# Kernel optimization log

Hardware: AMD Instinct MI355X
Metric: run time of the kernel (lower is better)

## Reference

```python
import jax, jax.numpy as jnp
import numpy as np

B, S, C = 16, 1024, 8
V, D, E, H, R = 50257, 512, 8, 512, 32
F, RT, CD, Q = 1024, 512, 64, 128
EPS = 1e-6


def _normalize(x):
    n = jnp.maximum(jnp.linalg.norm(x, axis=-1, keepdims=True), EPS)
    return x / n


def _fake_quantize(x):
    # F.normalize then straight-through int8 quant on the unit vector
    xn = _normalize(x)
    q = jnp.clip(jnp.round(xn * 127.0), -127.0, 127.0)
    return xn + jax.lax.stop_gradient(q / 127.0 - xn)


def setup_inputs() -> dict:
    key = jax.random.key(0)
    ks = iter(jax.random.split(key, 64))

    def w(shape, s=0.02):
        return (jax.random.normal(next(ks), shape, dtype=jnp.float32) * s)

    inp = {}
    inp['prefix_tokens'] = jax.random.randint(next(ks), (B, S), 0, V, dtype=jnp.int32)
    inp['chunk_inputs'] = jax.random.randint(next(ks), (B, C), 0, V, dtype=jnp.int32)
    inp['chunk_targets'] = jax.random.randint(next(ks), (B, C), 0, V, dtype=jnp.int32)
    inp['next_chunk_tokens'] = jax.random.randint(next(ks), (B, C), 0, V, dtype=jnp.int32)

    inp['emb'] = w((V, D))
    # stacked per-expert AffineExpert params
    inp['Wa'] = w((E, D, H)); inp['ba'] = jnp.zeros((E, H), jnp.float32)
    inp['Wg'] = w((E, D, R)); inp['bg'] = jnp.zeros((E, R), jnp.float32)
    inp['Wu'] = w((E, D, H)); inp['bu'] = jnp.zeros((E, H), jnp.float32)
    inp['u_mat'] = w((E, H, R)); inp['v_mat'] = w((E, H, R))
    inp['Wp'] = w((E, H, F)); inp['bp'] = jnp.zeros((E, F), jnp.float32)
    # gate MLP
    inp['Wg1'] = w((D, D)); inp['bg1'] = jnp.zeros((D,), jnp.float32)
    inp['Wg2'] = w((D, E)); inp['bg2'] = jnp.zeros((E,), jnp.float32)
    # query / target / key / code-expansion / write-code
    inp['Wq'] = w((F, Q)); inp['bq'] = jnp.zeros((Q,), jnp.float32)
    inp['Wt1'] = w((2 * D, RT)); inp['bt1'] = jnp.zeros((RT,), jnp.float32)
    inp['Wt2'] = w((RT, RT)); inp['bt2'] = jnp.zeros((RT,), jnp.float32)
    inp['Wk'] = w((RT, Q)); inp['bk'] = jnp.zeros((Q,), jnp.float32)
    inp['Web'] = w((CD, RT))  # expansion_basis (no bias)
    inp['Wwc'] = w((F, CD)); inp['bwc'] = jnp.zeros((CD,), jnp.float32)
    # ctx MLP
    inp['Wc1'] = w((2 * F, F)); inp['bc1'] = jnp.zeros((F,), jnp.float32)
    inp['Wc2'] = w((F, F)); inp['bc2'] = jnp.zeros((F,), jnp.float32)
    # chunk decoder
    inp['chunk_pos'] = w((C, F))
    inp['Wci'] = w((D + F, F)); inp['bci'] = jnp.zeros((F,), jnp.float32)
    inp['Wm1'] = w((F, F)); inp['bm1'] = jnp.zeros((F,), jnp.float32)
    inp['Wm2'] = w((F, F)); inp['bm2'] = jnp.zeros((F,), jnp.float32)
    inp['Wlm'] = w((F, V)); inp['blm'] = jnp.zeros((V,), jnp.float32)
    return inp


def _expert_scan(x, Wa, ba, Wg, bg, Wu, bu, u_mat, v_mat):
    # x: [B,S,D]; precompute all per-step projections as one big GEMM each,
    # leading axis = time for lax.scan. A,U: [S,E,B,H], G: [S,E,B,R]
    A = jax.nn.sigmoid(jnp.einsum('bsd,edh->sebh', x, Wa) + ba[None, :, None, :])
    G = jnp.einsum('bsd,edr->sebr', x, Wg) + bg[None, :, None, :]
    U = jnp.einsum('bsd,edh->sebh', x, Wu) + bu[None, :, None, :]

    def step(state, inp):  # state: [E,B,H]
        a, g, u = inp
        low = jnp.einsum('ebh,ehr->ebr', state, v_mat) * g
        state = a * state + u + jnp.einsum('ebr,ehr->ebh', low, u_mat)
        return state, None

    state0 = jnp.zeros((E, B, H), x.dtype)
    state, _ = jax.lax.scan(step, state0, (A, G, U))
    return state  # [E,B,H]


def reference(prefix_tokens, chunk_inputs, chunk_targets, next_chunk_tokens,
              emb, Wa, ba, Wg, bg, Wu, bu, u_mat, v_mat, Wp, bp,
              Wg1, bg1, Wg2, bg2, Wq, bq, Wt1, bt1, Wt2, bt2, Wk, bk,
              Web, Wwc, bwc, Wc1, bc1, Wc2, bc2,
              chunk_pos, Wci, bci, Wm1, bm1, Wm2, bm2, Wlm, blm):
    # ---- encode_prefix ----
    prefix_emb = emb[prefix_tokens]                       # [B,S,D]
    summary = prefix_emb.mean(axis=1)                     # [B,D]
    gate_probs = jax.nn.softmax(jax.nn.silu(summary @ Wg1 + bg1) @ Wg2 + bg2, axis=-1)  # [B,E]
    states = _expert_scan(prefix_emb, Wa, ba, Wg, bg, Wu, bu, u_mat, v_mat)             # [E,B,H]
    proj = jnp.einsum('ebh,ehf->ebf', states, Wp) + bp[:, None, :]                       # [E,B,F]
    fused = jnp.einsum('ebf,be->bf', proj, gate_probs)    # [B,F]

    # ---- query / target / key ----
    q_st = _fake_quantize(fused @ Wq + bq)                # [B,Q]
    chunk_emb = emb[chunk_targets].mean(axis=1)           # [B,D]
    next_emb = emb[next_chunk_tokens].mean(axis=1)        # [B,D]
    t_in = jnp.concatenate([chunk_emb, next_emb], axis=-1)
    target_state = _normalize(jax.nn.silu(t_in @ Wt1 + bt1) @ Wt2 + bt2)  # [B,RT]
    target_k_st = _fake_quantize(target_state @ Wk + bk)  # [B,Q]

    # ---- read_context (bank=None path -> zero read) ----
    zero_read = jnp.zeros_like(fused)
    c_in = jnp.concatenate([fused, zero_read], axis=-1)
    ctx = jax.nn.silu(c_in @ Wc1 + bc1) @ Wc2 + bc2       # [B,F]

    # ---- write_from_ctx ----
    write_codes = ctx @ Wwc + bwc                         # [B,CD]
    write_state = _normalize(write_codes @ Web)           # [B,RT]
    write_k_st = _fake_quantize(write_state @ Wk + bk)    # [B,Q]

    # ---- decode_chunk ----
    tok = emb[chunk_inputs]                               # [B,C,D]
    ctx_rep = jnp.broadcast_to(ctx[:, None, :], (B, C, F))
    hidden = jnp.concatenate([tok, ctx_rep], axis=-1) @ Wci + bci + chunk_pos[None]  # [B,C,F]
    hidden = jax.nn.silu(hidden @ Wm1 + bm1) @ Wm2 + bm2
    logits = hidden @ Wlm + blm                           # [B,C,V]

    # ---- losses ----
    logp = jax.nn.log_softmax(logits, axis=-1)
    token_loss = -jnp.take_along_axis(logp, chunk_targets[..., None], axis=-1)[..., 0]
    loss_nll = token_loss.mean()
    sim = (q_st @ target_k_st.T) / jnp.sqrt(jnp.float32(Q))  # [B,B]
    return logits, loss_nll, sim, write_k_st
```

## Files before the change

kernel.cpp:

```cpp
#include <hip/hip_runtime.h>
#include <math.h>

constexpr int BB = 16;
constexpr int SS = 1024;
constexpr int CC = 8;
constexpr int VV = 50257;
constexpr int DD = 512;
constexpr int EE = 8;
constexpr int HH = 512;
constexpr int RR = 32;
constexpr int FF = 1024;
constexpr int RTd = 512;
constexpr int CDd = 64;
constexpr int QQ = 128;
constexpr int SCH = 128;

typedef short bf16x8 __attribute__((ext_vector_type(8)));
typedef float f32x4 __attribute__((ext_vector_type(4)));

__device__ __forceinline__ float sigm(float x){ return 1.0f/(1.0f+expf(-x)); }

__device__ __forceinline__ unsigned short f2bf(float f){
  unsigned int u = __float_as_uint(f);
  u += 0x7fff + ((u>>16)&1);
  return (unsigned short)(u>>16);
}
__device__ __forceinline__ float bf2f(unsigned short h){
  return __uint_as_float(((unsigned int)h)<<16);
}

__device__ __forceinline__ void gload16(unsigned short* l, const unsigned short* g){
  __builtin_amdgcn_global_load_lds(
      (const __attribute__((address_space(1))) unsigned int*)(g),
      (__attribute__((address_space(3))) unsigned int*)(l), 16, 0, 0);
}

__global__ __launch_bounds__(256) void gather_pack(const int* __restrict__ toks,
    const float* __restrict__ emb, unsigned short* __restrict__ xp){
  int id = blockIdx.x*256 + threadIdx.x;
  int b = id >> 17;
  int rem = id & 131071;
  int c = rem >> 14;
  int rem2 = rem & 16383;
  int kc = rem2 >> 10;
  int pb = rem2 & 1023;
  int row = pb >> 3, q = pb & 7;
  int v = q ^ (row & 7);
  int kq = v >> 1, h = v & 1;
  int tok = toks[b*SS + c*128 + row];
  const float* src = emb + (size_t)tok*DD + kc*32 + kq*8;
  unsigned short o[8];
  #pragma unroll
  for (int j=0;j<8;j++){
    float f = src[j];
    unsigned short hi = f2bf(f);
    o[j] = h ? f2bf(f - bf2f(hi)) : hi;
  }
  ushort4* dst = (ushort4*)(xp + (size_t)id*8);
  dst[0] = make_ushort4(o[0],o[1],o[2],o[3]);
  dst[1] = make_ushort4(o[4],o[5],o[6],o[7]);
}

__global__ __launch_bounds__(512) void colsum_part(const int* __restrict__ toks,
    const float* __restrict__ emb, float* __restrict__ part){
  int b = blockIdx.y, j = blockIdx.x, d = threadIdx.x;
  float s = 0.f;
  for (int k=0;k<64;k++){
    int tok = toks[b*SS + j*64 + k];
    s += emb[(size_t)tok*DD + d];
  }
  part[(b*16 + j)*DD + d] = s;
}
__global__ __launch_bounds__(512) void colsum_final(const float* __restrict__ part,
                                                    float* __restrict__ summary){
  int b = blockIdx.x, d = threadIdx.x;
  float s = 0.f;
  for (int j=0;j<16;j++) s += part[(b*16 + j)*DD + d];
  summary[b*DD + d] = s * (1.0f/1024.0f);
}

__global__ __launch_bounds__(128) void gate_h1(const float* __restrict__ summary,
                                               const float* __restrict__ Wg1,
                                               const float* __restrict__ bg1,
                                               float* __restrict__ h1){
  int t = threadIdx.x; int j = blockIdx.x*128 + t;
  __shared__ float sm[16*512];
  for (int idx=t; idx<8192; idx+=128) sm[idx] = summary[idx];
  __syncthreads();
  float acc[16] = {0};
  for (int d=0; d<DD; d++){
    float w = Wg1[d*DD + j];
    #pragma unroll
    for (int b2=0;b2<16;b2++) acc[b2] += sm[b2*DD + d]*w;
  }
  #pragma unroll
  for (int b2=0;b2<16;b2++){ float v = acc[b2] + bg1[j]; h1[b2*DD + j] = v*sigm(v); }
}
__global__ __launch_bounds__(128) void gate_probs_k(const float* __restrict__ h1,
                                                    const float* __restrict__ Wg2,
                                                    const float* __restrict__ bg2,
                                                    float* __restrict__ gate){
  int t = threadIdx.x;
  int b = t>>3, e = t&7;
  float acc = bg2[e];
  for (int d=0; d<DD; d++) acc += h1[b*DD + d]*Wg2[d*EE + e];
  __shared__ float lg[16][8];
  lg[b][e] = acc;
  __syncthreads();
  if (e==0){
    float m = -3.4e38f;
    for (int i=0;i<8;i++) m = fmaxf(m, lg[b][i]);
    float s = 0.f; float ex[8];
    for (int i=0;i<8;i++){ ex[i] = expf(lg[b][i]-m); s += ex[i]; }
    for (int i=0;i<8;i++) gate[b*EE + i] = ex[i]/s;
  }
}

__global__ __launch_bounds__(256) void convT_pack_au(const float* __restrict__ Wa,
    const float* __restrict__ Wu, unsigned short* __restrict__ WPackAU){
  const int bid = blockIdx.x;
  const int e = bid >> 5;
  const int au = (bid >> 4) & 1;
  const int kc = bid & 15;
  const float* W = (au ? Wu : Wa) + (size_t)e*DD*HH + (size_t)kc*32*HH;
  __shared__ float tw[32][513];
  const int t = threadIdx.x;
  for (int i=0;i<64;i++){
    int id = t + i*256;
    int c = id & 511, k = id >> 9;
    tw[k][c] = W[(size_t)k*HH + c];
  }
  __syncthreads();
  for (int i=0;i<16;i++){
    int slot = t + i*256;
    int wq = slot >> 10, rem = slot & 1023;
    int cf = rem >> 7, hl = (rem >> 6) & 1, lane = rem & 63;
    int col = wq*128 + cf*16 + (lane & 15);
    int kb = lane >> 4;
    unsigned short o[8];
    #pragma unroll
    for (int j=0;j<8;j++){
      float f = tw[kb*8 + j][col];
      unsigned short hi = f2bf(f);
      o[j] = hl ? f2bf(f - bf2f(hi)) : hi;
    }
    size_t dst = (size_t)(e*2+au)*524288 + (size_t)(wq*16 + kc)*8192
               + (size_t)(cf*2 + hl)*512 + lane*8;
    *(ushort4*)&WPackAU[dst]   = make_ushort4(o[0],o[1],o[2],o[3]);
    *(ushort4*)&WPackAU[dst+4] = make_ushort4(o[4],o[5],o[6],o[7]);
  }
}
__global__ __launch_bounds__(256) void convT_pack_g(const float* __restrict__ Wge,
    unsigned short* __restrict__ WPG){
  const int kc = blockIdx.x;
  __shared__ float tg[32][257];
  const int t = threadIdx.x;
  for (int i=0;i<32;i++){
    int id = t + i*256;
    int r = id & 31, k = (id >> 5) & 31, e = id >> 10;
    tg[k][e*32 + r] = Wge[((size_t)e*DD + kc*32 + k)*RR + r];
  }
  __syncthreads();
  for (int i=0;i<8;i++){
    int slot = t + i*256;
    int w = slot >> 8, rem = slot & 255;
    int cf = rem >> 7, hl = (rem >> 6) & 1, lane = rem & 63;
    int gcol = w*32 + cf*16 + (lane & 15);
    int kb = lane >> 4;
    unsigned short o[8];
    #pragma unroll
    for (int j=0;j<8;j++){
      float f = tg[kb*8 + j][gcol];
      unsigned short hi = f2bf(f);
      o[j] = hl ? f2bf(f - bf2f(hi)) : hi;
    }
    size_t dst = (((size_t)(w*16 + kc)*2 + cf)*2 + hl)*512 + lane*8;
    *(ushort4*)&WPG[dst]   = make_ushort4(o[0],o[1],o[2],o[3]);
    *(ushort4*)&WPG[dst+4] = make_ushort4(o[4],o[5],o[6],o[7]);
  }
}

__global__ __launch_bounds__(512, 2) void aug_scan(
    const unsigned short* __restrict__ xp,
    const unsigned short* __restrict__ WPackAU, const unsigned short* __restrict__ WPG,
    const float* __restrict__ ba, const float* __restrict__ bu, const float* __restrict__ bge,
    float* __restrict__ Aw, float* __restrict__ Uw, float* __restrict__ Gw,
    const float* __restrict__ Ar, const float* __restrict__ Ur, const float* __restrict__ Gr,
    const float* __restrict__ v_mat, const float* __restrict__ u_mat,
    float* __restrict__ states,
    int s0, int do_aug, int do_scan)
{
  __shared__ __align__(16) unsigned short lds[40960];
  const int t = threadIdx.x;
  const int xcd  = blockIdx.x & 7;
  const int slot = blockIdx.x >> 3;
  const int lane = t & 63, wv = t >> 6;

  if (slot < 16){
    if (!do_scan) return;
    const int e = xcd;
    const int b = slot;
    const int r = t & 31, grp = t >> 5;
    float* f     = (float*)lds;
    float* stf   = f;
    float* partf = f + 1024;
    float* lowf  = f + 1312;
    float* bufG  = f + 1536;
    float* bufA  = f + 2048;
    float* bufU  = f + 10240;
    float vreg[32];
    #pragma unroll
    for (int i=0;i<32;i++) vreg[i] = v_mat[((size_t)e*HH + grp*32 + i)*RR + r];
    float ureg[32];
    {
      const float4* up = (const float4*)(u_mat + ((size_t)e*HH + t)*RR);
      #pragma unroll
      for (int j=0;j<8;j++){
        float4 v4 = up[j];
        ureg[j*4+0]=v4.x; ureg[j*4+1]=v4.y; ureg[j*4+2]=v4.z; ureg[j*4+3]=v4.w;
      }
    }
    const size_t sbase  = ((size_t)e*BB + b)*HH + t;
    const size_t abase0 = ((size_t)e*BB + b)*SCH*HH;
    const size_t gbase0 = ((size_t)e*BB + b)*SCH*RR;

#define STAGE_S(BUF, BT) { \
    const float* As_ = Ar + abase0 + (size_t)(BT)*8*HH + wv*512; \
    const float* Us_ = Ur + abase0 + (size_t)(BT)*8*HH + wv*512; \
    float* Ad_ = bufA + (BUF)*4096 + wv*512; \
    float* Ud_ = bufU + (BUF)*4096 + wv*512; \
    gload16((unsigned short*)Ad_,       (const unsigned short*)(As_ + lane*4)); \
    gload16((unsigned short*)(Ad_+256), (const unsigned short*)(As_ + 256 + lane*4)); \
    gload16((unsigned short*)Ud_,       (const unsigned short*)(Us_ + lane*4)); \
    gload16((unsigned short*)(Ud_+256), (const unsigned short*)(Us_ + 256 + lane*4)); \
    if (wv == 0) gload16((unsigned short*)(bufG + (BUF)*256), \
                         (const unsigned short*)(Gr + gbase0 + (size_t)(BT)*256 + lane*4)); }

    float streg = states[sbase];
    stf[t] = streg;
    STAGE_S(0, 0)
    asm volatile("s_waitcnt vmcnt(0)" ::: "memory");
    __syncthreads();
    int cur = 0, pc = 0;
    for (int bt=0; bt<16; bt++){
      if (bt < 15) STAGE_S(cur^1, bt+1)
      for (int s8=0; s8<8; s8++){
        float a = bufA[cur*4096 + s8*512 + t];
        float u = bufU[cur*4096 + s8*512 + t];
        {
          const float* sp = &stf[pc*512 + grp*32];
          float p0=0.f,p1=0.f,p2=0.f,p3=0.f;
          #pragma unroll
          for (int i=0;i<8;i++){
            p0 += sp[i]    *vreg[i];
            p1 += sp[8+i]  *vreg[8+i];
            p2 += sp[16+i] *vreg[16+i];
            p3 += sp[24+i] *vreg[24+i];
          }
          float p = (p0+p1)+(p2+p3);
          p += __shfl_xor(p, 32, 64);
          if ((t & 32) == 0) partf[r*9 + (grp>>1)] = p;
        }
        __syncthreads();
        if (t < 32){
          float ss2 = 0.f;
          #pragma unroll
          for (int j=0;j<8;j++) ss2 += partf[t*9 + j];
          lowf[t] = ss2 * bufG[cur*256 + s8*32 + t];
        }
        __syncthreads();
        {
          float q0=0.f,q1=0.f,q2=0.f,q3=0.f;
          #pragma unroll
          for (int i=0;i<8;i++){
            q0 += lowf[i]   *ureg[i];
            q1 += lowf[8+i] *ureg[8+i];
            q2 += lowf[16+i]*ureg[16+i];
            q3 += lowf[24+i]*ureg[24+i];
          }
          streg = a*streg + u + ((q0+q1)+(q2+q3));
        }
        stf[(pc^1)*512 + t] = streg;
        pc ^= 1;
        __syncthreads();
      }
      asm volatile("s_waitcnt vmcnt(0)" ::: "memory");
      __syncthreads();
      cur ^= 1;
    }
#undef STAGE_S
    states[sbase] = streg;
    return;
  }

  if (!do_aug) return;
  const int cl15 = lane & 15;
  const int kb = lane >> 4;
  const int cix = s0 >> 7;

  if (slot < 48){
    const int e = xcd;
    const int idx = slot - 16;
    const int b = idx & 15;
    const int r0 = (idx >> 4) * 64;
    const unsigned short* xpc = xp + (((size_t)(b*8 + cix)) << 17);
    const int au = wv >> 2, wq = wv & 3;
    const unsigned short* wb = WPackAU + (size_t)(e*2+au)*524288 + (size_t)wq*16*8192;
    const int kcl_s = wv >> 1;
    const int halfr = wv & 1;

#define STAGE_Q(BUF, Q) { \
    const int kcq_ = (Q)*4 + kcl_s; \
    const unsigned short* src_ = xpc + kcq_*8192 + r0*64 + halfr*2048; \
    unsigned short* dst_ = lds + (BUF)*16384 + kcl_s*4096 + halfr*2048; \
    _Pragma("unroll") \
    for (int i_=0;i_<4;i_++) gload16(dst_ + i_*512, src_ + (size_t)(i_*64 + lane)*8); }

    STAGE_Q(0, 0)
    asm volatile("s_waitcnt vmcnt(0)" ::: "memory");
    __builtin_amdgcn_s_barrier();

    f32x4 acc[4][8] = {};
    int cur = 0;
    for (int q=0; q<4; q++){
      if (q < 3) STAGE_Q(cur^1, q+1)
      for (int kc2=0; kc2<4; kc2++){
        const int kc = q*4 + kc2;
        const unsigned short* xb = lds + cur*16384 + kc2*4096;
        bf16x8 ah[4], al[4];
        #pragma unroll
        for (int rf=0; rf<4; rf++){
          const int rloc = rf*16 + cl15;
          const int qh = (kb*2) ^ (rloc & 7);
          ah[rf] = *(const bf16x8*)&xb[rloc*64 + qh*8];
          al[rf] = *(const bf16x8*)&xb[rloc*64 + (qh^1)*8];
        }
        #pragma unroll
        for (int cf=0; cf<8; cf++){
          const unsigned short* fp = wb + ((size_t)kc*8 + cf)*1024 + lane*8;
          bf16x8 bh = *(const bf16x8*)fp;
          bf16x8 bl = *(const bf16x8*)(fp + 512);
          #pragma unroll
          for (int rf=0; rf<4; rf++){
            acc[rf][cf] = __builtin_amdgcn_mfma_f32_16x16x32_bf16(ah[rf], bh, acc[rf][cf], 0,0,0);
            acc[rf][cf] = __builtin_amdgcn_mfma_f32_16x16x32_bf16(ah[rf], bl, acc[rf][cf], 0,0,0);
            acc[rf][cf] = __builtin_amdgcn_mfma_f32_16x16x32_bf16(al[rf], bh, acc[rf][cf], 0,0,0);
          }
        }
      }
      asm volatile("s_waitcnt vmcnt(0)" ::: "memory");
      __builtin_amdgcn_s_barrier();
      cur ^= 1;
    }
#undef STAGE_Q
    const float* bias = au ? bu : ba;
    float* dst = (au ? Uw : Aw) + ((size_t)(e*BB + b)*SCH + r0)*HH;
    #pragma unroll
    for (int rf=0; rf<4; rf++){
      #pragma unroll
      for (int cf=0; cf<8; cf++){
        const int col = wq*128 + cf*16 + cl15;
        const float bv = bias[e*HH + col];
        #pragma unroll
        for (int i=0;i<4;i++){
          const int rloc = rf*16 + (lane>>4)*4 + i;
          float v = acc[rf][cf][i] + bv;
          if (!au) v = sigm(v);
          dst[(size_t)rloc*HH + col] = v;
        }
      }
    }
  } else {
    const int idx2 = slot - 48;
    const int b = (xcd << 1) | (idx2 & 1);
    const int r0 = (idx2 >> 1) * 32;
    const unsigned short* xpc = xp + (((size_t)(b*8 + cix)) << 17);
    {
      const int kc = wv;
      const unsigned short* src = xpc + kc*8192 + r0*64;
      unsigned short* dst = lds + kc*2048;
      #pragma unroll
      for (int i=0;i<4;i++)
        gload16(dst + i*512, src + (size_t)(i*64 + lane)*8);
    }
    __syncthreads();
    {
      const int kc = 8 + wv;
      const unsigned short* src = xpc + kc*8192 + r0*64;
      unsigned short* dst = lds + kc*2048;
      #pragma unroll
      for (int i=0;i<4;i++)
        gload16(dst + i*512, src + (size_t)(i*64 + lane)*8);
    }
    f32x4 acc[2][2] = {};
    const unsigned short* wb = WPG + (size_t)wv*32768;
    for (int half=0; half<2; half++){
      if (half) __syncthreads();
      for (int kc = half*8; kc < half*8 + 8; kc++){
        bf16x8 ah[2], al[2];
        #pragma unroll
        for (int rf=0; rf<2; rf++){
          const int rloc = rf*16 + cl15;
          const int qh = (kb*2) ^ (rloc & 7);
          ah[rf] = *(const bf16x8*)&lds[kc*2048 + rloc*64 + qh*8];
          al[rf] = *(const bf16x8*)&lds[kc*2048 + rloc*64 + (qh^1)*8];
        }
        #pragma unroll
        for (int cf=0; cf<2; cf++){
          const unsigned short* fp = wb + ((size_t)kc*2 + cf)*1024 + lane*8;
          bf16x8 bh = *(const bf16x8*)fp;
          bf16x8 bl = *(const bf16x8*)(fp + 512);
          #pragma unroll
          for (int rf=0; rf<2; rf++){
            acc[rf][cf] = __builtin_amdgcn_mfma_f32_16x16x32_bf16(ah[rf], bh, acc[rf][cf], 0,0,0);
            acc[rf][cf] = __builtin_amdgcn_mfma_f32_16x16x32_bf16(ah[rf], bl, acc[rf][cf], 0,0,0);
            acc[rf][cf] = __builtin_amdgcn_mfma_f32_16x16x32_bf16(al[rf], bh, acc[rf][cf], 0,0,0);
          }
        }
      }
    }
    #pragma unroll
    for (int rf=0; rf<2; rf++){
      #pragma unroll
      for (int cf=0; cf<2; cf++){
        const int gcol = wv*32 + cf*16 + cl15;
        const int ee = gcol >> 5, r = gcol & 31;
        const float bv = bge[ee*RR + r];
        #pragma unroll
        for (int i=0;i<4;i++){
          const int rloc = rf*16 + (lane>>4)*4 + i;
          Gw[((size_t)(ee*BB + b)*SCH + r0 + rloc)*RR + r] = acc[rf][cf][i] + bv;
        }
      }
    }
  }
}

__global__ __launch_bounds__(128) void proj_partial(const float* __restrict__ states,
    const float* __restrict__ Wp, const float* __restrict__ gate, float* __restrict__ pf){
  int fc = blockIdx.x, e = blockIdx.y, t = threadIdx.x;
  __shared__ float stl[16*512];
  for (int idx=t; idx<8192; idx+=128) stl[idx] = states[(size_t)e*8192 + idx];
  __syncthreads();
  int f = fc*128 + t;
  float acc[16] = {0};
  for (int h=0; h<HH; h++){
    float w = Wp[((size_t)e*HH + h)*FF + f];
    #pragma unroll
    for (int b2=0;b2<16;b2++) acc[b2] += stl[b2*HH + h]*w;
  }
  #pragma unroll
  for (int b2=0;b2<16;b2++) pf[((size_t)(e*16 + b2))*FF + f] = gate[b2*EE + e]*acc[b2];
}
__global__ __launch_bounds__(256) void fuse_reduce(const float* __restrict__ pf,
    const float* __restrict__ gate, const float* __restrict__ bp, float* __restrict__ fused){
  int idx = blockIdx.x*256 + threadIdx.x;
  int b = idx >> 10, f = idx & 1023;
  float s = 0.f;
  #pragma unroll
  for (int e=0;e<8;e++) s += pf[((size_t)(e*16 + b))*FF + f] + gate[b*EE + e]*bp[e*FF + f];
  fused[idx] = s;
}

__global__ __launch_bounds__(128) void fq_linear(const float* __restrict__ in, int Kin,
    const float* __restrict__ W, const float* __restrict__ bias, float* __restrict__ out){
  int b = blockIdx.x, t = threadIdx.x;
  __shared__ float xin[1024];
  __shared__ float red[2];
  for (int k=t;k<Kin;k+=128) xin[k] = in[(size_t)b*Kin + k];
  __syncthreads();
  float acc = bias[t];
  for (int k=0;k<Kin;k++) acc += xin[k]*W[k*QQ + t];
  float ss = acc*acc;
  #pragma unroll
  for (int off=32; off; off>>=1) ss += __shfl_xor(ss, off, 64);
  if ((t&63)==0) red[t>>6] = ss;
  __syncthreads();
  float n = fmaxf(sqrtf(red[0]+red[1]), 1e-6f);
  float xn = acc / n;
  float q = fminf(fmaxf(rintf(xn*127.0f), -127.0f), 127.0f) * (1.0f/127.0f);
  out[b*QQ + t] = q;
}

__global__ __launch_bounds__(512) void chunk_means(const int* __restrict__ ct,
    const int* __restrict__ nct, const float* __restrict__ emb, float* __restrict__ tin){
  int b = blockIdx.x, d = threadIdx.x;
  float ce=0.f, ne=0.f;
  for (int c=0;c<CC;c++){
    ce += emb[(size_t)ct[b*CC+c]*DD + d];
    ne += emb[(size_t)nct[b*CC+c]*DD + d];
  }
  tin[b*1024 + d] = ce*0.125f;
  tin[b*1024 + 512 + d] = ne*0.125f;
}

__global__ __launch_bounds__(512) void target_state_kernel(const float* __restrict__ tin,
    const float* __restrict__ Wt1, const float* __restrict__ bt1,
    const float* __restrict__ Wt2, const float* __restrict__ bt2, float* __restrict__ outts){
  int b = blockIdx.x, t = threadIdx.x;
  __shared__ float xin[1024];
  __shared__ float h1[512];
  __shared__ float red[8];
  for (int k=t;k<1024;k+=512) xin[k] = tin[b*1024 + k];
  __syncthreads();
  float acc = bt1[t];
  for (int k=0;k<1024;k++) acc += xin[k]*Wt1[k*RTd + t];
  acc = acc*sigm(acc);
  h1[t] = acc;
  __syncthreads();
  float y = bt2[t];
  for (int k=0;k<512;k++) y += h1[k]*Wt2[k*RTd + t];
  float ss = y*y;
  #pragma unroll
  for (int off=32; off; off>>=1) ss += __shfl_xor(ss, off, 64);
  if ((t&63)==0) red[t>>6] = ss;
  __syncthreads();
  float tot = 0.f;
  #pragma unroll
  for (int i=0;i<8;i++) tot += red[i];
  float n = fmaxf(sqrtf(tot), 1e-6f);
  outts[b*RTd + t] = y/n;
}

__global__ __launch_bounds__(512) void write_state_kernel(const float* __restrict__ ctx,
    const float* __restrict__ Wwc, const float* __restrict__ bwc,
    const float* __restrict__ Web, float* __restrict__ wsn){
  int b = blockIdx.x, t = threadIdx.x;
  __shared__ float cx[1024];
  __shared__ float wc[64];
  __shared__ float red[8];
  for (int k=t;k<1024;k+=512) cx[k] = ctx[b*FF + k];
  __syncthreads();
  if (t < 64){
    float a = bwc[t];
    for (int k=0;k<1024;k++) a += cx[k]*Wwc[k*CDd + t];
    wc[t] = a;
  }
  __syncthreads();
  float y = 0.f;
  for (int k=0;k<64;k++) y += wc[k]*Web[k*RTd + t];
  float ss = y*y;
  #pragma unroll
  for (int off=32; off; off>>=1) ss += __shfl_xor(ss, off, 64);
  if ((t&63)==0) red[t>>6] = ss;
  __syncthreads();
  float tot = 0.f;
  #pragma unroll
  for (int i=0;i<8;i++) tot += red[i];
  float n = fmaxf(sqrtf(tot), 1e-6f);
  wsn[b*RTd + t] = y/n;
}

__global__ __launch_bounds__(256) void sim_kernel(const float* __restrict__ q,
    const float* __restrict__ k, float* __restrict__ out){
  int t = threadIdx.x;
  int i = t>>4, j = t&15;
  float s = 0.f;
  for (int c=0;c<QQ;c++) s += q[i*QQ + c]*k[j*QQ + c];
  out[t] = s / sqrtf(128.0f);
}

__global__ __launch_bounds__(256) void build_xcat(const int* __restrict__ ci,
    const float* __restrict__ emb, const float* __restrict__ ctx, float* __restrict__ xcat){
  int idx = blockIdx.x*256 + threadIdx.x;
  int row = idx / 1536, k = idx % 1536;
  float v = (k < DD) ? emb[(size_t)ci[row]*DD + k] : ctx[(row>>3)*FF + (k - DD)];
  xcat[idx] = v;
}

__global__ __launch_bounds__(256) void gemm_part(const float* __restrict__ X,
    const float* __restrict__ W, float* __restrict__ part,
    int K, int KS, int M){
  const int t = threadIdx.x;
  const int col = blockIdx.x*64 + (t & 63);
  const int r0 = blockIdx.y*16;
  const int ks = blockIdx.z;
  const int rg = t >> 6;
  const int kslice = K / KS;
  const int kbeg = ks*kslice;
  __shared__ float xs[16][65];
  float acc[4] = {};
  for (int k0=kbeg; k0<kbeg+kslice; k0+=64){
    #pragma unroll
    for (int i=0;i<4;i++){
      int id = t + i*256;
      int row = id >> 6, kk = id & 63;
      xs[row][kk] = X[(size_t)(r0+row)*K + k0 + kk];
    }
    __syncthreads();
    #pragma unroll 8
    for (int kk=0; kk<64; kk++){
      float w = W[(size_t)(k0+kk)*FF + col];
      #pragma unroll
      for (int i=0;i<4;i++) acc[i] += xs[rg*4+i][kk]*w;
    }
    __syncthreads();
  }
  #pragma unroll
  for (int i=0;i<4;i++)
    part[((size_t)ks*M + r0 + rg*4 + i)*FF + col] = acc[i];
}
__global__ __launch_bounds__(256) void gemm_combine(const float* __restrict__ part,
    const float* __restrict__ bias, const float* __restrict__ pos,
    float* __restrict__ outp, int KS, int M, int act){
  int idx = blockIdx.x*256 + threadIdx.x;
  int row = idx >> 10, col = idx & 1023;
  float v = bias[col];
  for (int k=0;k<KS;k++) v += part[(size_t)k*M*FF + idx];
  if (pos) v += pos[(row & 7)*FF + col];
  if (act) v = v*sigm(v);
  outp[idx] = v;
}

__global__ __launch_bounds__(256) void split_h(const float* __restrict__ hsrc,
    unsigned short* __restrict__ hh, unsigned short* __restrict__ hl){
  int idx = blockIdx.x*256 + threadIdx.x;
  float f = hsrc[idx];
  unsigned short h = f2bf(f);
  hh[idx] = h;
  hl[idx] = f2bf(f - bf2f(h));
}

__global__ __launch_bounds__(256) void logits_mfma(
    const unsigned short* __restrict__ hh, const unsigned short* __restrict__ hl,
    const float* __restrict__ Wlm, const float* __restrict__ blm,
    float* __restrict__ out){
  const int t = threadIdx.x;
  const int lane = t & 63, w = t >> 6;
  const int cb = blockIdx.x * 64;
  __shared__ __align__(16) unsigned short xsh[8*128*8];
  __shared__ __align__(16) unsigned short xsl[8*128*8];
  __shared__ __align__(16) unsigned short wsh[8*64*8];
  __shared__ __align__(16) unsigned short wsl[8*64*8];
  f32x4 acc[2][4] = {};
  for (int kc=0; kc<16; kc++){
    const int k0 = kc*64;
    #pragma unroll
    for (int i=0;i<4;i++){
      int id = t + i*256;
      int kq = id & 7, row = id >> 3;
      int pb = row*8 + (kq ^ (row&7));
      *(uint4*)&xsh[pb*8] = *(const uint4*)(hh + (size_t)row*FF + k0 + kq*8);
      *(uint4*)&xsl[pb*8] = *(const uint4*)(hl + (size_t)row*FF + k0 + kq*8);
    }
    #pragma unroll
    for (int i=0;i<2;i++){
      int id = t + i*256;
      int cc = id & 63, kq = id >> 6;
      int c = cb + cc; if (c >= VV) c = VV - 1;
      unsigned short h8[8], l8[8];
      #pragma unroll
      for (int j=0;j<8;j++){
        float f = Wlm[(size_t)(k0 + kq*8 + j)*VV + c];
        unsigned short h = f2bf(f);
        h8[j] = h;
        l8[j] = f2bf(f - bf2f(h));
      }
      int pb = kq*64 + cc;
      *(ushort4*)&wsh[pb*8]   = make_ushort4(h8[0],h8[1],h8[2],h8[3]);
      *(ushort4*)&wsh[pb*8+4] = make_ushort4(h8[4],h8[5],h8[6],h8[7]);
      *(ushort4*)&wsl[pb*8]   = make_ushort4(l8[0],l8[1],l8[2],l8[3]);
      *(ushort4*)&wsl[pb*8+4] = make_ushort4(l8[4],l8[5],l8[6],l8[7]);
    }
    __syncthreads();
    #pragma unroll
    for (int ks=0; ks<2; ks++){
      const int kq4 = ks*4 + (lane>>4);
      const int rr0 = w*32 + (lane&15);
      const int rr1 = rr0 + 16;
      bf16x8 ah0 = *(const bf16x8*)&xsh[(rr0*8 + (kq4^(rr0&7)))*8];
      bf16x8 ah1 = *(const bf16x8*)&xsh[(rr1*8 + (kq4^(rr1&7)))*8];
      bf16x8 al0 = *(const bf16x8*)&xsl[(rr0*8 + (kq4^(rr0&7)))*8];
      bf16x8 al1 = *(const bf16x8*)&xsl[(rr1*8 + (kq4^(rr1&7)))*8];
      #pragma unroll
      for (int cf=0; cf<4; cf++){
        const int cc = cf*16 + (lane&15);
        bf16x8 bh = *(const bf16x8*)&wsh[(kq4*64 + cc)*8];
        bf16x8 bl = *(const bf16x8*)&wsl[(kq4*64 + cc)*8];
        acc[0][cf] = __builtin_amdgcn_mfma_f32_16x16x32_bf16(ah0, bh, acc[0][cf], 0,0,0);
        acc[0][cf] = __builtin_amdgcn_mfma_f32_16x16x32_bf16(ah0, bl, acc[0][cf], 0,0,0);
        acc[0][cf] = __builtin_amdgcn_mfma_f32_16x16x32_bf16(al0, bh, acc[0][cf], 0,0,0);
        acc[1][cf] = __builtin_amdgcn_mfma_f32_16x16x32_bf16(ah1, bh, acc[1][cf], 0,0,0);
        acc[1][cf] = __builtin_amdgcn_mfma_f32_16x16x32_bf16(ah1, bl, acc[1][cf], 0,0,0);
        acc[1][cf] = __builtin_amdgcn_mfma_f32_16x16x32_bf16(al1, bh, acc[1][cf], 0,0,0);
      }
    }
    __syncthreads();
  }
  const int cl = lane & 15;
  const int r4 = (lane >> 4) * 4;
  #pragma unroll
  for (int rf=0; rf<2; rf++){
    #pragma unroll
    for (int cf=0; cf<4; cf++){
      int c = cb + cf*16 + cl;
      if (c >= VV) continue;
      float bb = blm[c];
      #pragma unroll
      for (int i=0;i<4;i++){
        int row = w*32 + rf*16 + r4 + i;
        out[(size_t)row*VV + c] = acc[rf][cf][i] + bb;
      }
    }
  }
}

__global__ __launch_bounds__(512) void softmax_nll(const float* __restrict__ logits,
    const int* __restrict__ tgt, float* __restrict__ tl){
  const int row = blockIdx.x;
  const float* p = logits + (size_t)row*VV;
  const int t = threadIdx.x;
  float m = -3.4e38f, s = 0.f;
  for (int c=t; c<VV; c+=512){
    float v = p[c];
    if (v > m){ s = s*expf(m - v) + 1.0f; m = v; }
    else s += expf(v - m);
  }
  #pragma unroll
  for (int off=32; off; off>>=1){
    float m2 = __shfl_xor(m, off, 64);
    float s2 = __shfl_xor(s, off, 64);
    float mn = fmaxf(m, m2);
    s = s*expf(m - mn) + s2*expf(m2 - mn);
    m = mn;
  }
  __shared__ float ms[8], ssh[8];
  if ((t&63)==0){ ms[t>>6] = m; ssh[t>>6] = s; }
  __syncthreads();
  if (t==0){
    float M = ms[0], S = ssh[0];
    for (int i=1;i<8;i++){
      float mn = fmaxf(M, ms[i]);
      S = S*expf(M-mn) + ssh[i]*expf(ms[i]-mn);
      M = mn;
    }
    tl[row] = M + logf(S) - p[tgt[row]];
  }
}
__global__ __launch_bounds__(128) void loss_reduce(const float* __restrict__ tl,
                                                   float* __restrict__ out){
  int t = threadIdx.x;
  float v = tl[t];
  #pragma unroll
  for (int off=32; off; off>>=1) v += __shfl_xor(v, off, 64);
  __shared__ float r2[2];
  if ((t&63)==0) r2[t>>6] = v;
  __syncthreads();
  if (t==0) out[0] = (r2[0]+r2[1]) * (1.0f/128.0f);
}

extern "C" void kernel_launch(void* const* d_in, const int* in_sizes, int n_in,
                              void* d_out, int out_size, void* d_ws, size_t ws_size,
                              hipStream_t stream){
  (void)in_sizes; (void)n_in; (void)out_size;
  const int*  prefix = (const int*)d_in[0];
  const int*  cinp   = (const int*)d_in[1];
  const int*  ctgt   = (const int*)d_in[2];
  const int*  nctk   = (const int*)d_in[3];
  const float* emb  = (const float*)d_in[4];
  const float* Wa   = (const float*)d_in[5];
  const float* ba   = (const float*)d_in[6];
  const float* Wge  = (const float*)d_in[7];
  const float* bge  = (const float*)d_in[8];
  const float* Wu   = (const float*)d_in[9];
  const float* bu   = (const float*)d_in[10];
  const float* u_mat= (const float*)d_in[11];
  const float* v_mat= (const float*)d_in[12];
  const float* Wp   = (const float*)d_in[13];
  const float* bp   = (const float*)d_in[14];
  const float* Wg1  = (const float*)d_in[15];
  const float* bg1  = (const float*)d_in[16];
  const float* Wg2  = (const float*)d_in[17];
  const float* bg2  = (const float*)d_in[18];
  const float* Wq   = (const float*)d_in[19];
  const float* bq   = (const float*)d_in[20];
  const float* Wt1  = (const float*)d_in[21];
  const float* bt1  = (const float*)d_in[22];
  const float* Wt2  = (const float*)d_in[23];
  const float* bt2  = (const float*)d_in[24];
  const float* Wk   = (const float*)d_in[25];
  const float* bk   = (const float*)d_in[26];
  const float* Web  = (const float*)d_in[27];
  const float* Wwc  = (const float*)d_in[28];
  const float* bwc  = (const float*)d_in[29];
  const float* Wc1  = (const float*)d_in[30];
  const float* bc1  = (const float*)d_in[31];
  const float* Wc2  = (const float*)d_in[32];
  const float* bc2  = (const float*)d_in[33];
  const float* cpos = (const float*)d_in[34];
  const float* Wci  = (const float*)d_in[35];
  const float* bci  = (const float*)d_in[36];
  const float* Wm1  = (const float*)d_in[37];
  const float* bm1  = (const float*)d_in[38];
  const float* Wm2  = (const float*)d_in[39];
  const float* bm2  = (const float*)d_in[40];
  const float* Wlm  = (const float*)d_in[41];
  const float* blm  = (const float*)d_in[42];

  float* ws = (float*)d_ws;
  size_t off = 0;
  unsigned short* xp = (unsigned short*)(ws + off); off += (size_t)BB*SS*DD;
  float* Abuf0  = ws + off; off += (size_t)SCH*EE*BB*HH;
  float* Ubuf0  = ws + off; off += (size_t)SCH*EE*BB*HH;
  float* Gbuf0  = ws + off; off += (size_t)SCH*EE*BB*RR;
  float* statesb= ws + off; off += (size_t)EE*BB*HH;
  float* partb  = ws + off; off += (size_t)BB*16*DD;
  float* summb  = ws + off; off += (size_t)BB*DD;
  float* h1b    = ws + off; off += (size_t)BB*DD;
  float* gateb  = ws + off; off += (size_t)BB*EE;
  float* pfb    = ws + off; off += (size_t)EE*BB*FF;
  float* fusedb = ws + off; off += (size_t)BB*FF;
  float* qstb   = ws + off; off += (size_t)BB*QQ;
  float* tinb   = ws + off; off += (size_t)BB*2*DD;
  float* tstb   = ws + off; off += (size_t)BB*RTd;
  float* tkb    = ws + off; off += (size_t)BB*QQ;
  float* ctxb   = ws + off; off += (size_t)BB*FF;
  float* hctxb  = ws + off; off += (size_t)BB*FF;
  float* wsnb   = ws + off; off += (size_t)BB*RTd;
  float* xcatb  = ws + off; off += (size_t)BB*CC*(DD+FF);
  float* hid1b  = ws + off; off += (size_t)BB*CC*FF;
  float* h2b    = ws + off; off += (size_t)BB*CC*FF;
  float* hidb   = ws + off; off += (size_t)BB*CC*FF;
  float* tlb    = ws + off; off += (size_t)BB*CC;
  float* ppart  = ws + off; off += (size_t)4*BB*CC*FF;
  unsigned short* WPackAU = (unsigned short*)(ws + off); off += (size_t)EE*DD*HH*2;
  unsigned short* WPG     = (unsigned short*)(ws + off); off += (size_t)EE*DD*RR;
  unsigned short* hhb  = (unsigned short*)(ws + off); off += (size_t)BB*CC*FF/2;
  unsigned short* hlb  = (unsigned short*)(ws + off); off += (size_t)BB*CC*FF/2;
  float* Abuf1  = ws + off; off += (size_t)SCH*EE*BB*HH;
  float* Ubuf1  = ws + off; off += (size_t)SCH*EE*BB*HH;
  float* Gbuf1  = ws + off; off += (size_t)SCH*EE*BB*RR;
  const bool fused = ws_size >= off * sizeof(float);

  float* out = (float*)d_out;
  const size_t LOGITS_OFF = 0;
  const size_t LOSS_OFF = (size_t)BB*CC*VV;
  const size_t SIM_OFF  = LOSS_OFF + 1;
  const size_t WK_OFF   = SIM_OFF + (size_t)BB*BB;

  convT_pack_au<<<256, 256, 0, stream>>>(Wa, Wu, WPackAU);
  convT_pack_g<<<16, 256, 0, stream>>>(Wge, WPG);

  gather_pack<<<8192, 256, 0, stream>>>(prefix, emb, xp);
  colsum_part<<<dim3(16,16), 512, 0, stream>>>(prefix, emb, partb);
  colsum_final<<<16, 512, 0, stream>>>(partb, summb);
  gate_h1<<<4, 128, 0, stream>>>(summb, Wg1, bg1, h1b);
  gate_probs_k<<<1, 128, 0, stream>>>(h1b, Wg2, bg2, gateb);

  hipMemsetAsync(statesb, 0, (size_t)EE*BB*HH*sizeof(float), stream);

  if (fused){
    for (int c=0; c<=8; c++){
      int da = (c<8) ? 1 : 0;
      int dscn = (c>=1) ? 1 : 0;
      float* Aw = (c&1) ? Abuf1 : Abuf0;
      float* Uw = (c&1) ? Ubuf1 : Ubuf0;
      float* Gw = (c&1) ? Gbuf1 : Gbuf0;
      const float* Ar = ((c-1)&1) ? Abuf1 : Abuf0;
      const float* Ur = ((c-1)&1) ? Ubuf1 : Ubuf0;
      const float* Gr = ((c-1)&1) ? Gbuf1 : Gbuf0;
      int grid = da ? 448 : 128;
      aug_scan<<<grid, 512, 0, stream>>>(xp, WPackAU, WPG, ba, bu, bge,
          Aw, Uw, Gw, Ar, Ur, Gr, v_mat, u_mat, statesb,
          c*SCH, da, dscn);
    }
  } else {
    for (int c=0; c<8; c++){
      aug_scan<<<448, 512, 0, stream>>>(xp, WPackAU, WPG, ba, bu, bge,
          Abuf0, Ubuf0, Gbuf0, Abuf0, Ubuf0, Gbuf0, v_mat, u_mat, statesb,
          c*SCH, 1, 0);
      aug_scan<<<128, 512, 0, stream>>>(xp, WPackAU, WPG, ba, bu, bge,
          Abuf0, Ubuf0, Gbuf0, Abuf0, Ubuf0, Gbuf0, v_mat, u_mat, statesb,
          c*SCH, 0, 1);
    }
  }

  proj_partial<<<dim3(8,8), 128, 0, stream>>>(statesb, Wp, gateb, pfb);
  fuse_reduce<<<64, 256, 0, stream>>>(pfb, gateb, bp, fusedb);

  fq_linear<<<16, 128, 0, stream>>>(fusedb, FF, Wq, bq, qstb);
  chunk_means<<<16, 512, 0, stream>>>(ctgt, nctk, emb, tinb);
  target_state_kernel<<<16, 512, 0, stream>>>(tinb, Wt1, bt1, Wt2, bt2, tstb);
  fq_linear<<<16, 128, 0, stream>>>(tstb, RTd, Wk, bk, tkb);

  gemm_part<<<dim3(16,1,4), 256, 0, stream>>>(fusedb, Wc1, ppart, FF, 4, 16);
  gemm_combine<<<64, 256, 0, stream>>>(ppart, bc1, nullptr, hctxb, 4, 16, 1);
  gemm_part<<<dim3(16,1,4), 256, 0, stream>>>(hctxb, Wc2, ppart, FF, 4, 16);
  gemm_combine<<<64, 256, 0, stream>>>(ppart, bc2, nullptr, ctxb, 4, 16, 0);

  write_state_kernel<<<16, 512, 0, stream>>>(ctxb, Wwc, bwc, Web, wsnb);
  fq_linear<<<16, 128, 0, stream>>>(wsnb, RTd, Wk, bk, out + WK_OFF);
  sim_kernel<<<1, 256, 0, stream>>>(qstb, tkb, out + SIM_OFF);

  build_xcat<<<768, 256, 0, stream>>>(cinp, emb, ctxb, xcatb);
  gemm_part<<<dim3(16,8,4), 256, 0, stream>>>(xcatb, Wci, ppart, DD+FF, 4, 128);
  gemm_combine<<<512, 256, 0, stream>>>(ppart, bci, cpos, hid1b, 4, 128, 0);
  gemm_part<<<dim3(16,8,4), 256, 0, stream>>>(hid1b, Wm1, ppart, FF, 4, 128);
  gemm_combine<<<512, 256, 0, stream>>>(ppart, bm1, nullptr, h2b, 4, 128, 1);
  gemm_part<<<dim3(16,8,4), 256, 0, stream>>>(h2b, Wm2, ppart, FF, 4, 128);
  gemm_combine<<<512, 256, 0, stream>>>(ppart, bm2, nullptr, hidb, 4, 128, 0);

  split_h<<<512, 256, 0, stream>>>(hidb, hhb, hlb);
  logits_mfma<<<(VV+63)/64, 256, 0, stream>>>(hhb, hlb, Wlm, blm, out + LOGITS_OFF);

  softmax_nll<<<BB*CC, 512, 0, stream>>>(out + LOGITS_OFF, ctgt, tlb);
  loss_reduce<<<1, 128, 0, stream>>>(tlb, out + LOSS_OFF);
}
```

Baseline: 1.703 ms.

## Rebalance scan/aug slot mapping, drop scan barrier, split proj and ctx GEMM K, stage Wlm via LDS

```diff
diff --git a/kernel.cpp b/kernel.cpp
--- a/kernel.cpp
+++ b/kernel.cpp
@@ -196,18 +196,22 @@
   const int slot = blockIdx.x >> 3;
   const int lane = t & 63, wv = t >> 6;
 
-  if (slot < 16){
+  int scan_b = -1;
+  if (slot < 8) scan_b = slot;
+  else if (slot >= 32 && slot < 40) scan_b = slot - 24;
+
+  if (scan_b >= 0){
     if (!do_scan) return;
     const int e = xcd;
-    const int b = slot;
+    const int b = scan_b;
     const int r = t & 31, grp = t >> 5;
     float* f     = (float*)lds;
     float* stf   = f;
     float* partf = f + 1024;
     float* lowf  = f + 1312;
-    float* bufG  = f + 1536;
-    float* bufA  = f + 2048;
-    float* bufU  = f + 10240;
+    float* bufG  = f + 1568;
+    float* bufA  = f + 2080;
+    float* bufU  = f + 10272;
     float vreg[32];
     #pragma unroll
     for (int i=0;i<32;i++) vreg[i] = v_mat[((size_t)e*HH + grp*32 + i)*RR + r];
@@ -259,24 +263,24 @@
           }
           float p = (p0+p1)+(p2+p3);
           p += __shfl_xor(p, 32, 64);
-          if ((t & 32) == 0) partf[r*9 + (grp>>1)] = p;
+          if ((t & 32) == 0) partf[r*9 + wv] = p;
         }
         __syncthreads();
-        if (t < 32){
+        if (lane < 32){
           float ss2 = 0.f;
           #pragma unroll
-          for (int j=0;j<8;j++) ss2 += partf[t*9 + j];
-          lowf[t] = ss2 * bufG[cur*256 + s8*32 + t];
+          for (int j=0;j<8;j++) ss2 += partf[lane*9 + j];
+          lowf[wv*32 + lane] = ss2 * bufG[cur*256 + s8*32 + lane];
         }
-        __syncthreads();
         {
+          const float* lw = &lowf[wv*32];
           float q0=0.f,q1=0.f,q2=0.f,q3=0.f;
           #pragma unroll
           for (int i=0;i<8;i++){
-            q0 += lowf[i]   *ureg[i];
-            q1 += lowf[8+i] *ureg[8+i];
-            q2 += lowf[16+i]*ureg[16+i];
-            q3 += lowf[24+i]*ureg[24+i];
+            q0 += lw[i]   *ureg[i];
+            q1 += lw[8+i] *ureg[8+i];
+            q2 += lw[16+i]*ureg[16+i];
+            q3 += lw[24+i]*ureg[24+i];
           }
           streg = a*streg + u + ((q0+q1)+(q2+q3));
         }
@@ -298,11 +302,14 @@
   const int kb = lane >> 4;
   const int cix = s0 >> 7;
 
-  if (slot < 48){
+  int auidx = -1;
+  if (slot >= 8 && slot < 32) auidx = slot - 8;
+  else if (slot >= 40 && slot < 48) auidx = 24 + (slot - 40);
+
+  if (auidx >= 0){
     const int e = xcd;
-    const int idx = slot - 16;
-    const int b = idx & 15;
-    const int r0 = (idx >> 4) * 64;
+    const int b = auidx & 15;
+    const int r0 = (auidx >> 4) * 64;
     const unsigned short* xpc = xp + (((size_t)(b*8 + cix)) << 17);
     const int au = wv >> 2, wq = wv & 3;
     const unsigned short* wb = WPackAU + (size_t)(e*2+au)*524288 + (size_t)wq*16*8192;
@@ -438,19 +445,23 @@
 
 __global__ __launch_bounds__(128) void proj_partial(const float* __restrict__ states,
     const float* __restrict__ Wp, const float* __restrict__ gate, float* __restrict__ pf){
-  int fc = blockIdx.x, e = blockIdx.y, t = threadIdx.x;
-  __shared__ float stl[16*512];
-  for (int idx=t; idx<8192; idx+=128) stl[idx] = states[(size_t)e*8192 + idx];
+  int fc = blockIdx.x, e = blockIdx.y, ks = blockIdx.z, t = threadIdx.x;
+  __shared__ float stl[16*256];
+  for (int idx=t; idx<4096; idx+=128){
+    int b2 = idx >> 8, h = idx & 255;
+    stl[idx] = states[(size_t)e*8192 + b2*512 + ks*256 + h];
+  }
   __syncthreads();
   int f = fc*128 + t;
   float acc[16] = {0};
-  for (int h=0; h<HH; h++){
-    float w = Wp[((size_t)e*HH + h)*FF + f];
-    #pragma unroll
-    for (int b2=0;b2<16;b2++) acc[b2] += stl[b2*HH + h]*w;
-  }
-  #pragma unroll
-  for (int b2=0;b2<16;b2++) pf[((size_t)(e*16 + b2))*FF + f] = gate[b2*EE + e]*acc[b2];
+  for (int h=0; h<256; h++){
+    float w = Wp[((size_t)e*HH + ks*256 + h)*FF + f];
+    #pragma unroll
+    for (int b2=0;b2<16;b2++) acc[b2] += stl[b2*256 + h]*w;
+  }
+  #pragma unroll
+  for (int b2=0;b2<16;b2++)
+    pf[(((size_t)ks*EE + e)*16 + b2)*FF + f] = gate[b2*EE + e]*acc[b2];
 }
 __global__ __launch_bounds__(256) void fuse_reduce(const float* __restrict__ pf,
     const float* __restrict__ gate, const float* __restrict__ bp, float* __restrict__ fused){
@@ -458,7 +469,11 @@
   int b = idx >> 10, f = idx & 1023;
   float s = 0.f;
   #pragma unroll
-  for (int e=0;e<8;e++) s += pf[((size_t)(e*16 + b))*FF + f] + gate[b*EE + e]*bp[e*FF + f];
+  for (int e=0;e<8;e++){
+    s += gate[b*EE + e]*bp[e*FF + f];
+    s += pf[((size_t)(e*16 + b))*FF + f];
+    s += pf[((size_t)((8+e)*16 + b))*FF + f];
+  }
   fused[idx] = s;
 }
 
@@ -632,6 +647,7 @@
   __shared__ __align__(16) unsigned short xsl[8*128*8];
   __shared__ __align__(16) unsigned short wsh[8*64*8];
   __shared__ __align__(16) unsigned short wsl[8*64*8];
+  __shared__ float wt[64][65];
   f32x4 acc[2][4] = {};
   for (int kc=0; kc<16; kc++){
     const int k0 = kc*64;
@@ -644,14 +660,21 @@
       *(uint4*)&xsl[pb*8] = *(const uint4*)(hl + (size_t)row*FF + k0 + kq*8);
     }
     #pragma unroll
+    for (int i=0;i<16;i++){
+      int id = t + i*256;
+      int col = id & 63, krow = id >> 6;
+      int c = cb + col; if (c >= VV) c = VV - 1;
+      wt[krow][col] = Wlm[(size_t)(k0 + krow)*VV + c];
+    }
+    __syncthreads();
+    #pragma unroll
     for (int i=0;i<2;i++){
       int id = t + i*256;
       int cc = id & 63, kq = id >> 6;
-      int c = cb + cc; if (c >= VV) c = VV - 1;
       unsigned short h8[8], l8[8];
       #pragma unroll
       for (int j=0;j<8;j++){
-        float f = Wlm[(size_t)(k0 + kq*8 + j)*VV + c];
+        float f = wt[kq*8 + j][cc];
         unsigned short h = f2bf(f);
         h8[j] = h;
         l8[j] = f2bf(f - bf2f(h));
@@ -808,7 +831,7 @@
   float* summb  = ws + off; off += (size_t)BB*DD;
   float* h1b    = ws + off; off += (size_t)BB*DD;
   float* gateb  = ws + off; off += (size_t)BB*EE;
-  float* pfb    = ws + off; off += (size_t)EE*BB*FF;
+  float* pfb    = ws + off; off += (size_t)2*EE*BB*FF;
   float* fusedb = ws + off; off += (size_t)BB*FF;
   float* qstb   = ws + off; off += (size_t)BB*QQ;
   float* tinb   = ws + off; off += (size_t)BB*2*DD;
@@ -822,7 +845,7 @@
   float* h2b    = ws + off; off += (size_t)BB*CC*FF;
   float* hidb   = ws + off; off += (size_t)BB*CC*FF;
   float* tlb    = ws + off; off += (size_t)BB*CC;
-  float* ppart  = ws + off; off += (size_t)4*BB*CC*FF;
+  float* ppart  = ws + off; off += (size_t)8*BB*CC*FF;
   unsigned short* WPackAU = (unsigned short*)(ws + off); off += (size_t)EE*DD*HH*2;
   unsigned short* WPG     = (unsigned short*)(ws + off); off += (size_t)EE*DD*RR;
   unsigned short* hhb  = (unsigned short*)(ws + off); off += (size_t)BB*CC*FF/2;
@@ -859,8 +882,7 @@
       const float* Ar = ((c-1)&1) ? Abuf1 : Abuf0;
       const float* Ur = ((c-1)&1) ? Ubuf1 : Ubuf0;
       const float* Gr = ((c-1)&1) ? Gbuf1 : Gbuf0;
-      int grid = da ? 448 : 128;
-      aug_scan<<<grid, 512, 0, stream>>>(xp, WPackAU, WPG, ba, bu, bge,
+      aug_scan<<<448, 512, 0, stream>>>(xp, WPackAU, WPG, ba, bu, bge,
           Aw, Uw, Gw, Ar, Ur, Gr, v_mat, u_mat, statesb,
           c*SCH, da, dscn);
     }
@@ -869,13 +891,13 @@
       aug_scan<<<448, 512, 0, stream>>>(xp, WPackAU, WPG, ba, bu, bge,
           Abuf0, Ubuf0, Gbuf0, Abuf0, Ubuf0, Gbuf0, v_mat, u_mat, statesb,
           c*SCH, 1, 0);
-      aug_scan<<<128, 512, 0, stream>>>(xp, WPackAU, WPG, ba, bu, bge,
+      aug_scan<<<448, 512, 0, stream>>>(xp, WPackAU, WPG, ba, bu, bge,
           Abuf0, Ubuf0, Gbuf0, Abuf0, Ubuf0, Gbuf0, v_mat, u_mat, statesb,
           c*SCH, 0, 1);
     }
   }
 
-  proj_partial<<<dim3(8,8), 128, 0, stream>>>(statesb, Wp, gateb, pfb);
+  proj_partial<<<dim3(8,8,2), 128, 0, stream>>>(statesb, Wp, gateb, pfb);
   fuse_reduce<<<64, 256, 0, stream>>>(pfb, gateb, bp, fusedb);
 
   fq_linear<<<16, 128, 0, stream>>>(fusedb, FF, Wq, bq, qstb);
@@ -883,10 +905,10 @@
   target_state_kernel<<<16, 512, 0, stream>>>(tinb, Wt1, bt1, Wt2, bt2, tstb);
   fq_linear<<<16, 128, 0, stream>>>(tstb, RTd, Wk, bk, tkb);
 
-  gemm_part<<<dim3(16,1,4), 256, 0, stream>>>(fusedb, Wc1, ppart, FF, 4, 16);
-  gemm_combine<<<64, 256, 0, stream>>>(ppart, bc1, nullptr, hctxb, 4, 16, 1);
-  gemm_part<<<dim3(16,1,4), 256, 0, stream>>>(hctxb, Wc2, ppart, FF, 4, 16);
-  gemm_combine<<<64, 256, 0, stream>>>(ppart, bc2, nullptr, ctxb, 4, 16, 0);
+  gemm_part<<<dim3(16,1,8), 256, 0, stream>>>(fusedb, Wc1, ppart, FF, 8, 16);
+  gemm_combine<<<64, 256, 0, stream>>>(ppart, bc1, nullptr, hctxb, 8, 16, 1);
+  gemm_part<<<dim3(16,1,8), 256, 0, stream>>>(hctxb, Wc2, ppart, FF, 8, 16);
+  gemm_combine<<<64, 256, 0, stream>>>(ppart, bc2, nullptr, ctxb, 8, 16, 0);
 
   write_state_kernel<<<16, 512, 0, stream>>>(ctxb, Wwc, bwc, Web, wsnb);
   fq_linear<<<16, 128, 0, stream>>>(wsnb, RTd, Wk, bk, out + WK_OFF);
```

After: 1.962 ms. +15.2%, slower.
